# Optimization experiments

Hardware: AMD Instinct MI355X
Metric: run time of the kernel (lower is better)

Reference implementation:

```python
import jax, jax.numpy as jnp
import numpy as np


def setup_inputs() -> dict:
    key = jax.random.key(0)
    k1, k2 = jax.random.split(key)
    b, d = 8192, 256
    x = jax.random.normal(k1, (b, d), dtype=jnp.float32)
    dc = jax.random.uniform(k2, (b, d), dtype=jnp.float32)
    dc_param = jnp.array([0.05], dtype=jnp.float32)
    return {"x": x, "dc": dc, "dc_param": dc_param}


def reference(x, dc, dc_param):
    # Faithful to torch: sim[i,j] = 1 / mean_k[(1-p)*(x[i,k]-x[j,k])^2
    #                                        + p*exp(1-dc[i,k])*exp(1-dc[j,k])]
    # Expanded to GEMMs to avoid the O(b^2*d) broadcast intermediate:
    #   mean_k (x_i - x_j)^2 = (|x_i|^2 + |x_j|^2 - 2 x_i.x_j) / d
    #   mean_k e_i[k] e_j[k] = (e_i . e_j) / d,  e = exp(1 - dc)
    b, d = x.shape
    p = dc_param[0]
    sq = jnp.sum(x * x, axis=1)                      # (b,)
    msd = (sq[:, None] + sq[None, :] - 2.0 * (x @ x.T)) / d  # (b,b)
    e = jnp.exp(1.0 - dc)                            # (b,d)
    mker = (e @ e.T) / d                             # (b,b)
    sim = 1.0 / ((1.0 - p) * msd + p * mker)
    eye = jnp.eye(b, dtype=x.dtype)
    return sim * (1.0 - eye) + eye
```

## Files before the change

kernel.cpp:

```cpp
#include <hip/hip_runtime.h>
#include <hip/hip_bf16.h>

typedef __attribute__((ext_vector_type(8))) __bf16 bf16x8;
typedef __attribute__((ext_vector_type(4))) float  f32x4;

constexpr int NROW = 8192;
constexpr int DDIM = 256;
constexpr int KDIM = 512;
constexpr int BM = 256, BN = 128, BK = 64;
constexpr int NT = KDIM / BK;
constexpr int ABYTES = BM * BK * 2;
constexpr int BBYTES = BN * BK * 2;
constexpr int BUFBYTES = ABYTES + BBYTES;
constexpr int NBUF = 3;
constexpr int LDS_TOTAL = NBUF * BUFBYTES;

__device__ __forceinline__ void gload_lds16(const void* g, void* l) {
  __builtin_amdgcn_global_load_lds(
      (const __attribute__((address_space(1))) void*)g,
      (__attribute__((address_space(3))) void*)l, 16, 0, 0);
}

__global__ __launch_bounds__(256) void prep_kernel(
    const float* __restrict__ x, const float* __restrict__ dc,
    const float* __restrict__ pparm,
    __hip_bfloat16* __restrict__ P, float* __restrict__ s)
{
  const int row = blockIdx.x;
  const int t   = threadIdx.x;
  const float xv = x[(size_t)row * DDIM + t];
  const float ev = __expf(1.0f - dc[(size_t)row * DDIM + t]);
  P[(size_t)row * KDIM + t]        = __float2bfloat16(xv);
  P[(size_t)row * KDIM + DDIM + t] = __float2bfloat16(ev);

  float v = xv * xv;
  #pragma unroll
  for (int off = 32; off > 0; off >>= 1) v += __shfl_down(v, off, 64);
  __shared__ float red[4];
  const int lane = t & 63, wid = t >> 6;
  if (lane == 0) red[wid] = v;
  __syncthreads();
  if (t == 0) {
    const float p = pparm[0];
    s[row] = (1.0f - p) * (1.0f / (float)DDIM) * (red[0] + red[1] + red[2] + red[3]);
  }
}

__global__ void __launch_bounds__(512, 2) adj_gemm(
    const __hip_bfloat16* __restrict__ P, const float* __restrict__ s,
    const float* __restrict__ pparm, float* __restrict__ out)
{
  extern __shared__ char lds[];

  const float p  = pparm[0];
  const float cx = -2.0f * (1.0f - p) / (float)DDIM;
  const float ce = p / (float)DDIM;
  const float midscale = cx / ce;

  const int orig  = blockIdx.x;
  const int x     = orig & 7;
  const int local = orig >> 3;
  const int bi = x * 4 + (local & 3);
  const int bj = local >> 2;
  const int rowBase = bi * BM;
  const int colBase = bj * BN;

  const int tid  = threadIdx.x;
  const int lane = tid & 63;
  const int wid  = tid >> 6;
  const int wrow = (wid >> 1) * 64;
  const int wcol = (wid & 1) * 64;
  const int frow = lane & 15;
  const int kq   = lane >> 4;

  const char* Pc = (const char*)P;
  const char* gsrc[6];
  int ldst[6];
  #pragma unroll
  for (int j = 0; j < 4; ++j) {
    const int o  = (j * 512 + tid) * 16;
    const int r  = o >> 7;
    const int cb = (o & 127) ^ (((o >> 9) & 1) << 5);
    gsrc[j] = Pc + ((size_t)(rowBase + r) * KDIM) * 2 + cb;
    ldst[j] = o;
  }
  #pragma unroll
  for (int j = 0; j < 2; ++j) {
    const int o  = (j * 512 + tid) * 16;
    const int r  = o >> 7;
    const int cb = (o & 127) ^ (((o >> 9) & 1) << 5);
    gsrc[4 + j] = Pc + ((size_t)(colBase + r) * KDIM) * 2 + cb;
    ldst[4 + j] = ABYTES + o;
  }

  #pragma unroll
  for (int j = 0; j < 6; ++j) gload_lds16(gsrc[j],       lds + ldst[j]);
  #pragma unroll
  for (int j = 0; j < 6; ++j) gload_lds16(gsrc[j] + 128, lds + BUFBYTES + ldst[j]);

  f32x4 acc[4][4];
  #pragma unroll
  for (int m = 0; m < 4; ++m)
    #pragma unroll
    for (int n = 0; n < 4; ++n)
      acc[m][n] = (f32x4){0.f, 0.f, 0.f, 0.f};

  #pragma unroll
  for (int t = 0; t < NT; ++t) {
    if (t < NT - 1) asm volatile("s_waitcnt vmcnt(6)" ::: "memory");
    else            asm volatile("s_waitcnt vmcnt(0)" ::: "memory");
    asm volatile("s_barrier" ::: "memory");

    char* buf  = lds + (t % NBUF) * BUFBYTES;
    char* nbuf = lds + ((t + 2) % NBUF) * BUFBYTES;
    const int gadv = (t + 2) * (BK * 2);

    bf16x8 a[4][2], bb[4][2];
    #pragma unroll
    for (int m = 0; m < 4; ++m)
      #pragma unroll
      for (int ks = 0; ks < 2; ++ks) {
        const int row = wrow + m * 16 + frow;
        const int cb  = (ks * 64 + kq * 16) ^ (((row >> 2) & 1) << 5);
        a[m][ks] = *(const bf16x8*)(buf + row * 128 + cb);
      }
    #pragma unroll
    for (int n = 0; n < 2; ++n)
      #pragma unroll
      for (int ks = 0; ks < 2; ++ks) {
        const int row = wcol + n * 16 + frow;
        const int cb  = (ks * 64 + kq * 16) ^ (((row >> 2) & 1) << 5);
        bb[n][ks] = *(const bf16x8*)(buf + ABYTES + row * 128 + cb);
      }
    if (t + 2 < NT) {
      gload_lds16(gsrc[0] + gadv, nbuf + ldst[0]);
      gload_lds16(gsrc[1] + gadv, nbuf + ldst[1]);
      gload_lds16(gsrc[2] + gadv, nbuf + ldst[2]);
    }
    __builtin_amdgcn_s_setprio(1);
    #pragma unroll
    for (int m = 0; m < 4; ++m)
      #pragma unroll
      for (int n = 0; n < 2; ++n)
        #pragma unroll
        for (int ks = 0; ks < 2; ++ks)
          acc[m][n] = __builtin_amdgcn_mfma_f32_16x16x32_bf16(a[m][ks], bb[n][ks], acc[m][n], 0, 0, 0);
    __builtin_amdgcn_s_setprio(0);
    asm volatile("s_barrier" ::: "memory");

    #pragma unroll
    for (int n = 2; n < 4; ++n)
      #pragma unroll
      for (int ks = 0; ks < 2; ++ks) {
        const int row = wcol + n * 16 + frow;
        const int cb  = (ks * 64 + kq * 16) ^ (((row >> 2) & 1) << 5);
        bb[n][ks] = *(const bf16x8*)(buf + ABYTES + row * 128 + cb);
      }
    if (t + 2 < NT) {
      gload_lds16(gsrc[3] + gadv, nbuf + ldst[3]);
      gload_lds16(gsrc[4] + gadv, nbuf + ldst[4]);
      gload_lds16(gsrc[5] + gadv, nbuf + ldst[5]);
    }
    __builtin_amdgcn_s_setprio(1);
    #pragma unroll
    for (int m = 0; m < 4; ++m)
      #pragma unroll
      for (int n = 2; n < 4; ++n)
        #pragma unroll
        for (int ks = 0; ks < 2; ++ks)
          acc[m][n] = __builtin_amdgcn_mfma_f32_16x16x32_bf16(a[m][ks], bb[n][ks], acc[m][n], 0, 0, 0);
    __builtin_amdgcn_s_setprio(0);

    if (t == DDIM / BK - 1) {
      #pragma unroll
      for (int m = 0; m < 4; ++m)
        #pragma unroll
        for (int n = 0; n < 4; ++n)
          acc[m][n] *= midscale;
    }
  }

  #pragma unroll
  for (int m = 0; m < 4; ++m) {
    const int growb = rowBase + wrow + m * 16 + (lane >> 4) * 4;
    float srow[4];
    #pragma unroll
    for (int r = 0; r < 4; ++r) srow[r] = s[growb + r];
    #pragma unroll
    for (int n = 0; n < 4; ++n) {
      const int gcol = colBase + wcol + n * 16 + (lane & 15);
      const float scol = s[gcol];
      #pragma unroll
      for (int r = 0; r < 4; ++r) {
        const int grow = growb + r;
        const float denom = srow[r] + scol + ce * acc[m][n][r];
        const float val = (grow == gcol) ? 1.0f : __builtin_amdgcn_rcpf(denom);
        out[(size_t)grow * NROW + gcol] = val;
      }
    }
  }
}

extern "C" void kernel_launch(void* const* d_in, const int* in_sizes, int n_in,
                              void* d_out, int out_size, void* d_ws, size_t ws_size,
                              hipStream_t stream) {
  const float* x  = (const float*)d_in[0];
  const float* dc = (const float*)d_in[1];
  const float* pp = (const float*)d_in[2];
  float* out = (float*)d_out;

  __hip_bfloat16* P = (__hip_bfloat16*)d_ws;
  float* s = (float*)((char*)d_ws + (size_t)NROW * KDIM * 2);

  hipFuncSetAttribute(reinterpret_cast<const void*>(adj_gemm),
                      hipFuncAttributeMaxDynamicSharedMemorySize, LDS_TOTAL);

  prep_kernel<<<NROW, 256, 0, stream>>>(x, dc, pp, P, s);
  adj_gemm<<<(NROW / BM) * (NROW / BN), 512, LDS_TOTAL, stream>>>(P, s, pp, out);
}
```

Baseline: 106.4 us.

## Enlarge GEMM tile to 256x256 with double-buffered interleaved LDS staging

Widens the block tile from 256x128 to 256x256, with each of the 8 waves computing a 128x64 sub-tile. Triple buffering becomes double buffering over 64KB tiles, with a new XOR swizzle and global-to-LDS loads spread across four MFMA phases per K step. The aim is more operand reuse per LDS byte and fewer global reloads of the packed operand matrix. In exchange, accumulator register pressure doubles and 128KB of LDS per block likely limits the kernel to one resident block per CU, while the large fp32 output store still dominates total traffic.

```diff
diff --git a/kernel.cpp b/kernel.cpp
--- a/kernel.cpp
+++ b/kernel.cpp
@@ -7,13 +7,10 @@
 constexpr int NROW = 8192;
 constexpr int DDIM = 256;
 constexpr int KDIM = 512;
-constexpr int BM = 256, BN = 128, BK = 64;
+constexpr int BM = 256, BN = 256, BK = 64;
 constexpr int NT = KDIM / BK;
-constexpr int ABYTES = BM * BK * 2;
-constexpr int BBYTES = BN * BK * 2;
-constexpr int BUFBYTES = ABYTES + BBYTES;
-constexpr int NBUF = 3;
-constexpr int LDS_TOTAL = NBUF * BUFBYTES;
+constexpr int TILEBYTES = 65536;
+constexpr int LDS_TOTAL = 2 * TILEBYTES;
 
 __device__ __forceinline__ void gload_lds16(const void* g, void* l) {
   __builtin_amdgcn_global_load_lds(
@@ -58,9 +55,9 @@
   const float midscale = cx / ce;
 
   const int orig  = blockIdx.x;
-  const int x     = orig & 7;
+  const int xcd   = orig & 7;
   const int local = orig >> 3;
-  const int bi = x * 4 + (local & 3);
+  const int bi = xcd * 4 + (local & 3);
   const int bj = local >> 2;
   const int rowBase = bi * BM;
   const int colBase = bj * BN;
@@ -68,132 +65,149 @@
   const int tid  = threadIdx.x;
   const int lane = tid & 63;
   const int wid  = tid >> 6;
-  const int wrow = (wid >> 1) * 64;
-  const int wcol = (wid & 1) * 64;
+  const int wmrow = (wid >> 2) * 128;
+  const int wnrow = (wid & 3) * 64;
   const int frow = lane & 15;
   const int kq   = lane >> 4;
 
+  const int colb0 = (kq * 16)      ^ ((frow & 7) << 4);
+  const int colb1 = (64 + kq * 16) ^ ((frow & 7) << 4);
+
+  const int r0   = tid >> 3;
+  const int cb   = (tid * 16) & 127;
+  const int cbsw = cb ^ ((r0 & 7) << 4);
   const char* Pc = (const char*)P;
-  const char* gsrc[6];
-  int ldst[6];
-  #pragma unroll
-  for (int j = 0; j < 4; ++j) {
-    const int o  = (j * 512 + tid) * 16;
-    const int r  = o >> 7;
-    const int cb = (o & 127) ^ (((o >> 9) & 1) << 5);
-    gsrc[j] = Pc + ((size_t)(rowBase + r) * KDIM) * 2 + cb;
-    ldst[j] = o;
-  }
-  #pragma unroll
-  for (int j = 0; j < 2; ++j) {
-    const int o  = (j * 512 + tid) * 16;
-    const int r  = o >> 7;
-    const int cb = (o & 127) ^ (((o >> 9) & 1) << 5);
-    gsrc[4 + j] = Pc + ((size_t)(colBase + r) * KDIM) * 2 + cb;
-    ldst[4 + j] = ABYTES + o;
-  }
-
-  #pragma unroll
-  for (int j = 0; j < 6; ++j) gload_lds16(gsrc[j],       lds + ldst[j]);
-  #pragma unroll
-  for (int j = 0; j < 6; ++j) gload_lds16(gsrc[j] + 128, lds + BUFBYTES + ldst[j]);
-
-  f32x4 acc[4][4];
-  #pragma unroll
-  for (int m = 0; m < 4; ++m)
+  const char* gA = Pc + ((size_t)(rowBase + r0) * KDIM) * 2 + cbsw;
+  const char* gB = Pc + ((size_t)(colBase + r0) * KDIM) * 2 + cbsw;
+
+#define STAGE(kk, region) do {                                                 \
+    const char* _src = ((region) < 2 ? gB : gA) + ((region) & 1) * (128 * KDIM * 2) \
+                       + (kk) * (BK * 2);                                      \
+    char* _dst = lds + ((kk) & 1) * TILEBYTES                                  \
+                 + (((region) < 2 ? 32768 : 0) + ((region) & 1) * 16384)       \
+                 + tid * 16;                                                   \
+    gload_lds16(_src, _dst);                                                   \
+    gload_lds16(_src + 64 * KDIM * 2, _dst + 8192);                            \
+  } while (0)
+
+  STAGE(0, 0); STAGE(0, 1); STAGE(0, 2); STAGE(0, 3);
+  STAGE(1, 0); STAGE(1, 1);
+  asm volatile("s_waitcnt vmcnt(4)" ::: "memory");
+  asm volatile("s_barrier" ::: "memory");
+
+  f32x4 acc[8][4];
+  #pragma unroll
+  for (int m = 0; m < 8; ++m)
     #pragma unroll
     for (int n = 0; n < 4; ++n)
       acc[m][n] = (f32x4){0.f, 0.f, 0.f, 0.f};
 
+  bf16x8 a[4][2], b[4][2];
+
   #pragma unroll
   for (int t = 0; t < NT; ++t) {
-    if (t < NT - 1) asm volatile("s_waitcnt vmcnt(6)" ::: "memory");
-    else            asm volatile("s_waitcnt vmcnt(0)" ::: "memory");
-    asm volatile("s_barrier" ::: "memory");
-
-    char* buf  = lds + (t % NBUF) * BUFBYTES;
-    char* nbuf = lds + ((t + 2) % NBUF) * BUFBYTES;
-    const int gadv = (t + 2) * (BK * 2);
-
-    bf16x8 a[4][2], bb[4][2];
-    #pragma unroll
-    for (int m = 0; m < 4; ++m)
-      #pragma unroll
-      for (int ks = 0; ks < 2; ++ks) {
-        const int row = wrow + m * 16 + frow;
-        const int cb  = (ks * 64 + kq * 16) ^ (((row >> 2) & 1) << 5);
-        a[m][ks] = *(const bf16x8*)(buf + row * 128 + cb);
-      }
-    #pragma unroll
-    for (int n = 0; n < 2; ++n)
-      #pragma unroll
-      for (int ks = 0; ks < 2; ++ks) {
-        const int row = wcol + n * 16 + frow;
-        const int cb  = (ks * 64 + kq * 16) ^ (((row >> 2) & 1) << 5);
-        bb[n][ks] = *(const bf16x8*)(buf + ABYTES + row * 128 + cb);
-      }
-    if (t + 2 < NT) {
-      gload_lds16(gsrc[0] + gadv, nbuf + ldst[0]);
-      gload_lds16(gsrc[1] + gadv, nbuf + ldst[1]);
-      gload_lds16(gsrc[2] + gadv, nbuf + ldst[2]);
-    }
-    __builtin_amdgcn_s_setprio(1);
-    #pragma unroll
-    for (int m = 0; m < 4; ++m)
-      #pragma unroll
-      for (int n = 0; n < 2; ++n)
-        #pragma unroll
-        for (int ks = 0; ks < 2; ++ks)
-          acc[m][n] = __builtin_amdgcn_mfma_f32_16x16x32_bf16(a[m][ks], bb[n][ks], acc[m][n], 0, 0, 0);
-    __builtin_amdgcn_s_setprio(0);
-    asm volatile("s_barrier" ::: "memory");
-
-    #pragma unroll
-    for (int n = 2; n < 4; ++n)
-      #pragma unroll
-      for (int ks = 0; ks < 2; ++ks) {
-        const int row = wcol + n * 16 + frow;
-        const int cb  = (ks * 64 + kq * 16) ^ (((row >> 2) & 1) << 5);
-        bb[n][ks] = *(const bf16x8*)(buf + ABYTES + row * 128 + cb);
-      }
-    if (t + 2 < NT) {
-      gload_lds16(gsrc[3] + gadv, nbuf + ldst[3]);
-      gload_lds16(gsrc[4] + gadv, nbuf + ldst[4]);
-      gload_lds16(gsrc[5] + gadv, nbuf + ldst[5]);
-    }
-    __builtin_amdgcn_s_setprio(1);
-    #pragma unroll
-    for (int m = 0; m < 4; ++m)
-      #pragma unroll
-      for (int n = 2; n < 4; ++n)
-        #pragma unroll
-        for (int ks = 0; ks < 2; ++ks)
-          acc[m][n] = __builtin_amdgcn_mfma_f32_16x16x32_bf16(a[m][ks], bb[n][ks], acc[m][n], 0, 0, 0);
+    const char* buf  = lds + (t & 1) * TILEBYTES;
+    const char* bufB = buf + 32768;
+
+    #pragma unroll
+    for (int i = 0; i < 4; ++i) {
+      const int row = wmrow + i * 16 + frow;
+      a[i][0] = *(const bf16x8*)(buf + row * 128 + colb0);
+      a[i][1] = *(const bf16x8*)(buf + row * 128 + colb1);
+    }
+    #pragma unroll
+    for (int i = 0; i < 2; ++i) {
+      const int row = wnrow + i * 16 + frow;
+      b[i][0] = *(const bf16x8*)(bufB + row * 128 + colb0);
+      b[i][1] = *(const bf16x8*)(bufB + row * 128 + colb1);
+    }
+    if (t < 7) STAGE(t + 1, 2);
+    asm volatile("s_barrier" ::: "memory");
+    __builtin_amdgcn_s_setprio(1);
+    #pragma unroll
+    for (int i = 0; i < 4; ++i)
+      #pragma unroll
+      for (int jn = 0; jn < 2; ++jn)
+        #pragma unroll
+        for (int ks = 0; ks < 2; ++ks)
+          acc[i][jn] = __builtin_amdgcn_mfma_f32_16x16x32_bf16(a[i][ks], b[jn][ks], acc[i][jn], 0, 0, 0);
+    __builtin_amdgcn_s_setprio(0);
+    asm volatile("s_barrier" ::: "memory");
+
+    #pragma unroll
+    for (int i = 0; i < 2; ++i) {
+      const int row = wnrow + (2 + i) * 16 + frow;
+      b[2 + i][0] = *(const bf16x8*)(bufB + row * 128 + colb0);
+      b[2 + i][1] = *(const bf16x8*)(bufB + row * 128 + colb1);
+    }
+    if (t < 7) STAGE(t + 1, 3);
+    asm volatile("s_barrier" ::: "memory");
+    __builtin_amdgcn_s_setprio(1);
+    #pragma unroll
+    for (int i = 0; i < 4; ++i)
+      #pragma unroll
+      for (int jn = 0; jn < 2; ++jn)
+        #pragma unroll
+        for (int ks = 0; ks < 2; ++ks)
+          acc[i][2 + jn] = __builtin_amdgcn_mfma_f32_16x16x32_bf16(a[i][ks], b[2 + jn][ks], acc[i][2 + jn], 0, 0, 0);
+    __builtin_amdgcn_s_setprio(0);
+    asm volatile("s_barrier" ::: "memory");
+
+    #pragma unroll
+    for (int i = 0; i < 4; ++i) {
+      const int row = wmrow + (4 + i) * 16 + frow;
+      a[i][0] = *(const bf16x8*)(buf + row * 128 + colb0);
+      a[i][1] = *(const bf16x8*)(buf + row * 128 + colb1);
+    }
+    if (t < 6) STAGE(t + 2, 0);
+    asm volatile("s_barrier" ::: "memory");
+    __builtin_amdgcn_s_setprio(1);
+    #pragma unroll
+    for (int i = 0; i < 4; ++i)
+      #pragma unroll
+      for (int jn = 0; jn < 2; ++jn)
+        #pragma unroll
+        for (int ks = 0; ks < 2; ++ks)
+          acc[4 + i][2 + jn] = __builtin_amdgcn_mfma_f32_16x16x32_bf16(a[i][ks], b[2 + jn][ks], acc[4 + i][2 + jn], 0, 0, 0);
+    __builtin_amdgcn_s_setprio(0);
+    asm volatile("s_barrier" ::: "memory");
+
+    if (t < 6) STAGE(t + 2, 1);
+    __builtin_amdgcn_s_setprio(1);
+    #pragma unroll
+    for (int i = 0; i < 4; ++i)
+      #pragma unroll
+      for (int jn = 0; jn < 2; ++jn)
+        #pragma unroll
+        for (int ks = 0; ks < 2; ++ks)
+          acc[4 + i][jn] = __builtin_amdgcn_mfma_f32_16x16x32_bf16(a[i][ks], b[jn][ks], acc[4 + i][jn], 0, 0, 0);
     __builtin_amdgcn_s_setprio(0);
 
     if (t == DDIM / BK - 1) {
       #pragma unroll
-      for (int m = 0; m < 4; ++m)
+      for (int m = 0; m < 8; ++m)
         #pragma unroll
         for (int n = 0; n < 4; ++n)
           acc[m][n] *= midscale;
     }
+
+    if (t < 6)       asm volatile("s_waitcnt vmcnt(4)" ::: "memory");
+    else if (t == 6) asm volatile("s_waitcnt vmcnt(0)" ::: "memory");
+    if (t < 7)       asm volatile("s_barrier" ::: "memory");
   }
 
-  #pragma unroll
-  for (int m = 0; m < 4; ++m) {
-    const int growb = rowBase + wrow + m * 16 + (lane >> 4) * 4;
-    float srow[4];
-    #pragma unroll
-    for (int r = 0; r < 4; ++r) srow[r] = s[growb + r];
-    #pragma unroll
-    for (int n = 0; n < 4; ++n) {
-      const int gcol = colBase + wcol + n * 16 + (lane & 15);
-      const float scol = s[gcol];
+  const int rq = lane >> 4;
+  #pragma unroll
+  for (int n = 0; n < 4; ++n) {
+    const int gcol = colBase + wnrow + n * 16 + frow;
+    const float scol = s[gcol];
+    #pragma unroll
+    for (int m = 0; m < 8; ++m) {
+      const int growb = rowBase + wmrow + m * 16 + rq * 4;
       #pragma unroll
       for (int r = 0; r < 4; ++r) {
         const int grow = growb + r;
-        const float denom = srow[r] + scol + ce * acc[m][n][r];
+        const float denom = s[grow] + scol + ce * acc[m][n][r];
         const float val = (grow == gcol) ? 1.0f : __builtin_amdgcn_rcpf(denom);
         out[(size_t)grow * NROW + gcol] = val;
       }
```

Result: slower. 114.6 us (+7.7%).

## Make GEMM persistent over column tiles, overlapping epilogue stores with next tile

Applied to the files above, without the earlier changes.

The GEMM now launches 256 blocks, one per CU-sized slot. Each block owns a 256-row stripe and loops over 8 column tiles, streaming K-tiles continuously across tile boundaries with a triple-buffered LDS pipeline. Each tile's epilogue results are held in registers and written with nontemporal stores interleaved into the next tile's K-loop, which hides the large output write behind MFMA work. Row and column norm values are staged into LDS by async loads, and the swizzle is changed to a 3-bit XOR. The costs are more registers for the pending results, possible occupancy loss, and more intricate waitcnt bookkeeping.

```diff
diff --git a/kernel.cpp b/kernel.cpp
--- a/kernel.cpp
+++ b/kernel.cpp
@@ -8,12 +8,11 @@
 constexpr int DDIM = 256;
 constexpr int KDIM = 512;
 constexpr int BM = 256, BN = 128, BK = 64;
-constexpr int NT = KDIM / BK;
-constexpr int ABYTES = BM * BK * 2;
-constexpr int BBYTES = BN * BK * 2;
-constexpr int BUFBYTES = ABYTES + BBYTES;
-constexpr int NBUF = 3;
-constexpr int LDS_TOTAL = NBUF * BUFBYTES;
+constexpr int ABY = BM * BK * 2;
+constexpr int BBY = BN * BK * 2;
+constexpr int BUF = ABY + BBY;
+constexpr int SOFF = 3 * BUF;
+constexpr int LDS_TOTAL = SOFF + 1536;
 
 __device__ __forceinline__ void gload_lds16(const void* g, void* l) {
   __builtin_amdgcn_global_load_lds(
@@ -47,7 +46,7 @@
 }
 
 __global__ void __launch_bounds__(512, 2) adj_gemm(
-    const __hip_bfloat16* __restrict__ P, const float* __restrict__ s,
+    const __hip_bfloat16* __restrict__ P, const float* __restrict__ sG,
     const float* __restrict__ pparm, float* __restrict__ out)
 {
   extern __shared__ char lds[];
@@ -57,147 +56,178 @@
   const float ce = p / (float)DDIM;
   const float midscale = cx / ce;
 
-  const int orig  = blockIdx.x;
-  const int x     = orig & 7;
-  const int local = orig >> 3;
-  const int bi = x * 4 + (local & 3);
-  const int bj = local >> 2;
+  const int blk  = blockIdx.x;
+  const int bi   = blk >> 3;
+  const int colg = blk & 7;
   const int rowBase = bi * BM;
-  const int colBase = bj * BN;
 
   const int tid  = threadIdx.x;
   const int lane = tid & 63;
   const int wid  = tid >> 6;
-  const int wrow = (wid >> 1) * 64;
-  const int wcol = (wid & 1) * 64;
+  const int wmrow = (wid >> 1) * 64;
+  const int wnrow = (wid & 1) * 64;
   const int frow = lane & 15;
   const int kq   = lane >> 4;
 
-  const char* Pc = (const char*)P;
-  const char* gsrc[6];
-  int ldst[6];
-  #pragma unroll
-  for (int j = 0; j < 4; ++j) {
-    const int o  = (j * 512 + tid) * 16;
-    const int r  = o >> 7;
-    const int cb = (o & 127) ^ (((o >> 9) & 1) << 5);
-    gsrc[j] = Pc + ((size_t)(rowBase + r) * KDIM) * 2 + cb;
-    ldst[j] = o;
-  }
-  #pragma unroll
-  for (int j = 0; j < 2; ++j) {
-    const int o  = (j * 512 + tid) * 16;
-    const int r  = o >> 7;
-    const int cb = (o & 127) ^ (((o >> 9) & 1) << 5);
-    gsrc[4 + j] = Pc + ((size_t)(colBase + r) * KDIM) * 2 + cb;
-    ldst[4 + j] = ABYTES + o;
-  }
-
-  #pragma unroll
-  for (int j = 0; j < 6; ++j) gload_lds16(gsrc[j],       lds + ldst[j]);
-  #pragma unroll
-  for (int j = 0; j < 6; ++j) gload_lds16(gsrc[j] + 128, lds + BUFBYTES + ldst[j]);
-
-  f32x4 acc[4][4];
+  const int qr   = tid >> 3;
+  const int cbsw = ((tid & 7) * 16) ^ ((qr & 7) << 4);
+  const char* Pc  = (const char*)P;
+  const char* bA0 = Pc + (size_t)(rowBase + qr)      * 1024 + cbsw;
+  const char* bB0 = Pc + (size_t)(colg * 1024 + qr)  * 1024 + cbsw;
+  const int   d0  = tid * 16;
+
+#define STAGE(bufp, sub2, t2) do {                                          \
+    gload_lds16(bA0 +           (t2) * 128, (bufp) + d0);                   \
+    gload_lds16(bA0 + 65536 +   (t2) * 128, (bufp) + d0 + 8192);            \
+    gload_lds16(bA0 + 131072 +  (t2) * 128, (bufp) + d0 + 16384);           \
+    gload_lds16(bA0 + 196608 +  (t2) * 128, (bufp) + d0 + 24576);           \
+    gload_lds16(bB0 + (size_t)(sub2) * 131072 + (t2) * 128,                 \
+                (bufp) + ABY + d0);                                         \
+    gload_lds16(bB0 + 65536 + (size_t)(sub2) * 131072 + (t2) * 128,         \
+                (bufp) + ABY + d0 + 8192);                                  \
+  } while (0)
+
+  gload_lds16((const char*)sG + (size_t)rowBase * 4 + lane * 16,
+              lds + SOFF + lane * 16);
+  STAGE(lds,       0, 0);
+  STAGE(lds + BUF, 0, 1);
+  asm volatile("s_waitcnt vmcnt(6)" ::: "memory");
+  asm volatile("s_barrier" ::: "memory");
+
+  f32x4 acc[4][4], pend[4][4];
   #pragma unroll
   for (int m = 0; m < 4; ++m)
     #pragma unroll
     for (int n = 0; n < 4; ++n)
       acc[m][n] = (f32x4){0.f, 0.f, 0.f, 0.f};
 
-  #pragma unroll
-  for (int t = 0; t < NT; ++t) {
-    if (t < NT - 1) asm volatile("s_waitcnt vmcnt(6)" ::: "memory");
-    else            asm volatile("s_waitcnt vmcnt(0)" ::: "memory");
-    asm volatile("s_barrier" ::: "memory");
-
-    char* buf  = lds + (t % NBUF) * BUFBYTES;
-    char* nbuf = lds + ((t + 2) % NBUF) * BUFBYTES;
-    const int gadv = (t + 2) * (BK * 2);
-
-    bf16x8 a[4][2], bb[4][2];
+  float* outP = out + (size_t)(rowBase + wmrow + kq * 4) * NROW + wnrow + frow;
+  const float* sRow = (const float*)(lds + SOFF);
+  const float* sCol = (const float*)(lds + SOFF + 1024);
+
+  int cur = 0;
+  for (int sub = 0; sub < 8; ++sub) {
+    #pragma unroll
+    for (int t = 0; t < 8; ++t) {
+      char* buf  = lds + cur * BUF;
+      const int nx = (cur >= 1) ? cur - 1 : cur + 2;
+      char* nbuf = lds + nx * BUF;
+
+      if (sub > 0) {
+        const int m = t >> 1;
+        const int colPrev = (colg * 8 + sub - 1) * 128;
+        #pragma unroll
+        for (int nn = 0; nn < 2; ++nn) {
+          const int n = (t & 1) * 2 + nn;
+          #pragma unroll
+          for (int r = 0; r < 4; ++r)
+            __builtin_nontemporal_store(pend[m][n][r],
+                outP + (size_t)(m * 16 + r) * NROW + colPrev + n * 16);
+        }
+      }
+
+      if (t <= 5)       STAGE(nbuf, sub, t + 2);
+      else if (sub < 7) STAGE(nbuf, sub + 1, t - 6);
+      if (t == 4) {
+        if (lane < 32)
+          gload_lds16((const char*)sG + (size_t)((colg * 8 + sub) * 128) * 4 + lane * 16,
+                      lds + SOFF + 1024 + lane * 16);
+      }
+
+      bf16x8 a[4][2], b[2][2];
+      #pragma unroll
+      for (int m = 0; m < 4; ++m) {
+        const int r = wmrow + m * 16 + frow;
+        #pragma unroll
+        for (int ks = 0; ks < 2; ++ks)
+          a[m][ks] = *(const bf16x8*)(buf + r * 128 +
+                        ((ks * 64 + kq * 16) ^ ((r & 7) << 4)));
+      }
+      #pragma unroll
+      for (int n = 0; n < 2; ++n) {
+        const int r = wnrow + n * 16 + frow;
+        #pragma unroll
+        for (int ks = 0; ks < 2; ++ks)
+          b[n][ks] = *(const bf16x8*)(buf + ABY + r * 128 +
+                        ((ks * 64 + kq * 16) ^ ((r & 7) << 4)));
+      }
+      __builtin_amdgcn_s_setprio(1);
+      #pragma unroll
+      for (int m = 0; m < 4; ++m)
+        #pragma unroll
+        for (int n = 0; n < 2; ++n)
+          #pragma unroll
+          for (int ks = 0; ks < 2; ++ks)
+            acc[m][n] = __builtin_amdgcn_mfma_f32_16x16x32_bf16(a[m][ks], b[n][ks], acc[m][n], 0, 0, 0);
+      __builtin_amdgcn_s_setprio(0);
+
+      #pragma unroll
+      for (int n = 0; n < 2; ++n) {
+        const int r = wnrow + (2 + n) * 16 + frow;
+        #pragma unroll
+        for (int ks = 0; ks < 2; ++ks)
+          b[n][ks] = *(const bf16x8*)(buf + ABY + r * 128 +
+                        ((ks * 64 + kq * 16) ^ ((r & 7) << 4)));
+      }
+      __builtin_amdgcn_s_setprio(1);
+      #pragma unroll
+      for (int m = 0; m < 4; ++m)
+        #pragma unroll
+        for (int n = 0; n < 2; ++n)
+          #pragma unroll
+          for (int ks = 0; ks < 2; ++ks)
+            acc[m][2 + n] = __builtin_amdgcn_mfma_f32_16x16x32_bf16(a[m][ks], b[n][ks], acc[m][2 + n], 0, 0, 0);
+      __builtin_amdgcn_s_setprio(0);
+
+      if (t == 3) {
+        #pragma unroll
+        for (int m = 0; m < 4; ++m)
+          #pragma unroll
+          for (int n = 0; n < 4; ++n)
+            acc[m][n] *= midscale;
+      }
+
+      if (t == 7) {
+        const int colB = (colg * 8 + sub) * 128;
+        #pragma unroll
+        for (int m = 0; m < 4; ++m) {
+          const f32x4 sr = *(const f32x4*)&sRow[wmrow + m * 16 + kq * 4];
+          #pragma unroll
+          for (int n = 0; n < 4; ++n) {
+            const float sc = sCol[wnrow + n * 16 + frow];
+            const int gcol = colB + wnrow + n * 16 + frow;
+            #pragma unroll
+            for (int r = 0; r < 4; ++r) {
+              const int grow = rowBase + wmrow + m * 16 + kq * 4 + r;
+              const float denom = sr[r] + sc + ce * acc[m][n][r];
+              pend[m][n][r] = (grow == gcol) ? 1.0f : __builtin_amdgcn_rcpf(denom);
+            }
+            acc[m][n] = (f32x4){0.f, 0.f, 0.f, 0.f};
+          }
+        }
+      }
+
+      if (t == 4)                 asm volatile("s_waitcnt vmcnt(7)" ::: "memory");
+      else if (t <= 5)            asm volatile("s_waitcnt vmcnt(6)" ::: "memory");
+      else {
+        if (sub < 7)              asm volatile("s_waitcnt vmcnt(6)" ::: "memory");
+        else                      asm volatile("s_waitcnt vmcnt(0)" ::: "memory");
+      }
+      asm volatile("s_barrier" ::: "memory");
+      cur = (cur >= 2) ? 0 : cur + 1;
+    }
+  }
+
+  {
+    const int colPrev = (colg * 8 + 7) * 128;
     #pragma unroll
     for (int m = 0; m < 4; ++m)
       #pragma unroll
-      for (int ks = 0; ks < 2; ++ks) {
-        const int row = wrow + m * 16 + frow;
-        const int cb  = (ks * 64 + kq * 16) ^ (((row >> 2) & 1) << 5);
-        a[m][ks] = *(const bf16x8*)(buf + row * 128 + cb);
-      }
-    #pragma unroll
-    for (int n = 0; n < 2; ++n)
-      #pragma unroll
-      for (int ks = 0; ks < 2; ++ks) {
-        const int row = wcol + n * 16 + frow;
-        const int cb  = (ks * 64 + kq * 16) ^ (((row >> 2) & 1) << 5);
-        bb[n][ks] = *(const bf16x8*)(buf + ABYTES + row * 128 + cb);
-      }
-    if (t + 2 < NT) {
-      gload_lds16(gsrc[0] + gadv, nbuf + ldst[0]);
-      gload_lds16(gsrc[1] + gadv, nbuf + ldst[1]);
-      gload_lds16(gsrc[2] + gadv, nbuf + ldst[2]);
-    }
-    __builtin_amdgcn_s_setprio(1);
-    #pragma unroll
-    for (int m = 0; m < 4; ++m)
-      #pragma unroll
-      for (int n = 0; n < 2; ++n)
-        #pragma unroll
-        for (int ks = 0; ks < 2; ++ks)
-          acc[m][n] = __builtin_amdgcn_mfma_f32_16x16x32_bf16(a[m][ks], bb[n][ks], acc[m][n], 0, 0, 0);
-    __builtin_amdgcn_s_setprio(0);
-    asm volatile("s_barrier" ::: "memory");
-
-    #pragma unroll
-    for (int n = 2; n < 4; ++n)
-      #pragma unroll
-      for (int ks = 0; ks < 2; ++ks) {
-        const int row = wcol + n * 16 + frow;
-        const int cb  = (ks * 64 + kq * 16) ^ (((row >> 2) & 1) << 5);
-        bb[n][ks] = *(const bf16x8*)(buf + ABYTES + row * 128 + cb);
-      }
-    if (t + 2 < NT) {
-      gload_lds16(gsrc[3] + gadv, nbuf + ldst[3]);
-      gload_lds16(gsrc[4] + gadv, nbuf + ldst[4]);
-      gload_lds16(gsrc[5] + gadv, nbuf + ldst[5]);
-    }
-    __builtin_amdgcn_s_setprio(1);
-    #pragma unroll
-    for (int m = 0; m < 4; ++m)
-      #pragma unroll
-      for (int n = 2; n < 4; ++n)
-        #pragma unroll
-        for (int ks = 0; ks < 2; ++ks)
-          acc[m][n] = __builtin_amdgcn_mfma_f32_16x16x32_bf16(a[m][ks], bb[n][ks], acc[m][n], 0, 0, 0);
-    __builtin_amdgcn_s_setprio(0);
-
-    if (t == DDIM / BK - 1) {
-      #pragma unroll
-      for (int m = 0; m < 4; ++m)
-        #pragma unroll
-        for (int n = 0; n < 4; ++n)
-          acc[m][n] *= midscale;
-    }
-  }
-
-  #pragma unroll
-  for (int m = 0; m < 4; ++m) {
-    const int growb = rowBase + wrow + m * 16 + (lane >> 4) * 4;
-    float srow[4];
-    #pragma unroll
-    for (int r = 0; r < 4; ++r) srow[r] = s[growb + r];
-    #pragma unroll
-    for (int n = 0; n < 4; ++n) {
-      const int gcol = colBase + wcol + n * 16 + (lane & 15);
-      const float scol = s[gcol];
-      #pragma unroll
-      for (int r = 0; r < 4; ++r) {
-        const int grow = growb + r;
-        const float denom = srow[r] + scol + ce * acc[m][n][r];
-        const float val = (grow == gcol) ? 1.0f : __builtin_amdgcn_rcpf(denom);
-        out[(size_t)grow * NROW + gcol] = val;
-      }
-    }
+      for (int n = 0; n < 4; ++n)
+        #pragma unroll
+        for (int r = 0; r < 4; ++r)
+          __builtin_nontemporal_store(pend[m][n][r],
+              outP + (size_t)(m * 16 + r) * NROW + colPrev + n * 16);
   }
 }
 
@@ -216,5 +246,5 @@
                       hipFuncAttributeMaxDynamicSharedMemorySize, LDS_TOTAL);
 
   prep_kernel<<<NROW, 256, 0, stream>>>(x, dc, pp, P, s);
-  adj_gemm<<<(NROW / BM) * (NROW / BN), 512, LDS_TOTAL, stream>>>(P, s, pp, out);
-}
+  adj_gemm<<<256, 512, LDS_TOTAL, stream>>>(P, s, pp, out);
+}
```

Result: slower. 145.7 us (+36.9%).
